# Performance work log

Measured on AMD Instinct MI355X. Metric: run time of the kernel, lower is better.

## Reference

```python
import jax, jax.numpy as jnp
import numpy as np

EMBED_DIM = 256
N_HEADS = 1
NORM_FACTOR = float(np.sqrt(EMBED_DIM / N_HEADS))


def setup_inputs() -> dict:
    key = jax.random.key(0)
    ks = jax.random.split(key, 7)
    B, S, E = 4, 4096, EMBED_DIM
    scale = 1.0 / np.sqrt(E)
    x = jax.random.normal(ks[0], (B, S, E), dtype=jnp.float32)
    Wq = jax.random.normal(ks[1], (E, E), dtype=jnp.float32) * scale
    bq = jax.random.normal(ks[2], (E,), dtype=jnp.float32) * 0.01
    Wk = jax.random.normal(ks[3], (E, E), dtype=jnp.float32) * scale
    bk = jax.random.normal(ks[4], (E,), dtype=jnp.float32) * 0.01
    Wv = jax.random.normal(ks[5], (E, E), dtype=jnp.float32) * scale
    bv = jax.random.normal(ks[6], (E,), dtype=jnp.float32) * 0.01
    return {"x": x, "Wq": Wq, "bq": bq, "Wk": Wk, "bk": bk, "Wv": Wv, "bv": bv}


def reference(x, Wq, bq, Wk, bk, Wv, bv):
    # Linear projections (torch Linear: x @ W.T + b; W here stored as [in, out]-equivalent square)
    q = x @ Wq + bq  # [B, S, E]
    k = x @ Wk + bk  # [B, S, E]
    v = x @ Wv + bv  # [B, S, E]
    # Full attention scores [B, S, S], scaled by sqrt(embed_dim / n_heads)
    attn_scores = jnp.einsum('bse,bte->bst', q, k) / NORM_FACTOR
    attn_dist = jax.nn.softmax(attn_scores, axis=-1)
    pooled = jnp.einsum('bst,bte->bse', attn_dist, v)  # [B, S, E]
    return pooled.mean(axis=1, keepdims=True)  # [B, 1, E]
```

## Files before the change

kernel.cpp:

```cpp
#include <hip/hip_runtime.h>
#include <stdint.h>

#define SS 4096
#define EE 256
#define C2 0.0901684400555602f

typedef __bf16 bf16x8 __attribute__((ext_vector_type(8)));
typedef float  f32x4  __attribute__((ext_vector_type(4)));

#if __has_builtin(__builtin_amdgcn_exp2f)
#define EXP2(x) __builtin_amdgcn_exp2f(x)
#else
#define EXP2(x) exp2f(x)
#endif
#if __has_builtin(__builtin_amdgcn_rcpf)
#define RCP(x) __builtin_amdgcn_rcpf(x)
#else
#define RCP(x) (1.0f / (x))
#endif

__device__ __forceinline__ uint16_t bf16_rn(float f) {
  uint32_t u = __float_as_uint(f);
  uint32_t r = (u + 0x7fffu + ((u >> 16) & 1u)) >> 16;
  return (uint16_t)r;
}
__device__ __forceinline__ float bf2f(uint16_t h) {
  return __uint_as_float(((uint32_t)h) << 16);
}
__device__ __forceinline__ bf16x8 pack_bf8(float4 a, float4 b) {
  union { bf16x8 v; uint16_t u[8]; } r;
  r.u[0] = bf16_rn(a.x); r.u[1] = bf16_rn(a.y);
  r.u[2] = bf16_rn(a.z); r.u[3] = bf16_rn(a.w);
  r.u[4] = bf16_rn(b.x); r.u[5] = bf16_rn(b.y);
  r.u[6] = bf16_rn(b.z); r.u[7] = bf16_rn(b.w);
  return r.v;
}

__device__ __forceinline__ f32x4 mfma16(bf16x8 a, bf16x8 b, f32x4 c) {
  return __builtin_amdgcn_mfma_f32_16x16x32_bf16(a, b, c, 0, 0, 0);
}

template<int R>
__device__ __forceinline__ void stage_tile(const uint16_t* gsrc, char* lds, int tid) {
  constexpr int NPER = (R * 32) / 256;
  const int wave = tid >> 6;
  #pragma unroll
  for (int c = 0; c < NPER; ++c) {
    int chunk = c * 256 + tid;
    int r = chunk >> 5;
    int ccl = (chunk & 31) ^ (r & 31);
    const char* gp = (const char*)gsrc + (r * 32 + ccl) * 16;
    char* lp = lds + (c * 256 + wave * 64) * 16;
    __builtin_amdgcn_global_load_lds(
        (const __attribute__((address_space(1))) uint32_t*)(uintptr_t)gp,
        (__attribute__((address_space(3))) uint32_t*)(uintptr_t)lp,
        16, 0, 0);
  }
}

__device__ __forceinline__ bf16x8 read_frag(const char* lds, int row, int cc) {
  int ccp = cc ^ (row & 31);
  return *(const bf16x8*)(lds + (row * 32 + ccp) * 16);
}

__global__ void prep_kernel(const float* __restrict__ Wq, const float* __restrict__ Wk,
                            const float* __restrict__ Wv, uint16_t* __restrict__ wt,
                            float* __restrict__ zbase, float* __restrict__ out) {
  __shared__ float t[64][65];
  const int bid = blockIdx.x, tid = threadIdx.x;
  if (bid >= 48) {
    int idx = (bid - 48) * 256 + tid;
    float4 z = {0.f, 0.f, 0.f, 0.f};
    if (idx < 8192) ((float4*)zbase)[idx] = z;
    else ((float4*)out)[idx - 8192] = z;
    return;
  }
  const int mat = bid >> 4, tt = bid & 15;
  const int ib = (tt >> 2) * 64, ob = (tt & 3) * 64;
  const float* W = (mat == 0) ? Wq : (mat == 1) ? Wk : Wv;
  #pragma unroll
  for (int p = 0; p < 4; ++p) {
    int idx = p * 256 + tid;
    int r = idx >> 4, c4 = idx & 15;
    float4 f = *(const float4*)&W[(size_t)(ib + r) * 256 + ob + c4 * 4];
    t[r][c4 * 4 + 0] = f.x; t[r][c4 * 4 + 1] = f.y;
    t[r][c4 * 4 + 2] = f.z; t[r][c4 * 4 + 3] = f.w;
  }
  __syncthreads();
  #pragma unroll
  for (int p = 0; p < 4; ++p) {
    int idx = p * 256 + tid;
    int o = idx >> 4, i4 = idx & 15;
    ushort4 u;
    u.x = bf16_rn(t[i4 * 4 + 0][o]);
    u.y = bf16_rn(t[i4 * 4 + 1][o]);
    u.z = bf16_rn(t[i4 * 4 + 2][o]);
    u.w = bf16_rn(t[i4 * 4 + 3][o]);
    *(ushort4*)&wt[((size_t)mat * 256 + ob + o) * 256 + ib + i4 * 4] = u;
  }
}

__global__ __launch_bounds__(256, 2) void qkv_kernel(
    const float* __restrict__ x, const uint16_t* __restrict__ wt,
    const float* __restrict__ bq, const float* __restrict__ bk, const float* __restrict__ bv,
    uint16_t* __restrict__ qo, uint16_t* __restrict__ ko, uint16_t* __restrict__ vo) {
  __shared__ char wsm[2][32768];
  const int tid = threadIdx.x;
  const int lane = tid & 63, wave = tid >> 6, quad = lane >> 4, lr = lane & 15;
  const int m0 = (blockIdx.x >> 2) * 128;
  const int cchunk = blockIdx.x & 3;
  stage_tile<64>(wt + (size_t)(cchunk * 192) * 256, wsm[0], tid);
  const float* ab = x + (size_t)(m0 + wave * 32) * EE;
  bf16x8 a[2][8];
  #pragma unroll
  for (int ms = 0; ms < 2; ++ms)
    #pragma unroll
    for (int f = 0; f < 8; ++f) {
      const float* rp = ab + (size_t)(ms * 16 + lr) * EE + f * 32 + quad * 8;
      a[ms][f] = pack_bf8(*(const float4*)rp, *(const float4*)(rp + 4));
    }
  for (int nc = 0; nc < 3; ++nc) {
    __syncthreads();
    if (nc < 2)
      stage_tile<64>(wt + (size_t)(cchunk * 192 + (nc + 1) * 64) * 256, wsm[(nc + 1) & 1], tid);
    const char* tile = wsm[nc & 1];
    #pragma unroll
    for (int nt = 0; nt < 4; ++nt) {
      const int eg0 = cchunk * 192 + nc * 64 + nt * 16;
      const int mat = eg0 >> 8;
      const int e = (eg0 & 255) + lr;
      const float* bias = (mat == 0) ? bq : (mat == 1) ? bk : bv;
      uint16_t* outp = (mat == 0) ? qo : (mat == 1) ? ko : vo;
      bf16x8 bf[8];
      #pragma unroll
      for (int f = 0; f < 8; ++f) bf[f] = read_frag(tile, nt * 16 + lr, f * 4 + quad);
      f32x4 acc[2] = {};
      #pragma unroll
      for (int f = 0; f < 8; ++f)
        #pragma unroll
        for (int ms = 0; ms < 2; ++ms)
          acc[ms] = mfma16(a[ms][f], bf[f], acc[ms]);
      const float bsv = bias[e];
      #pragma unroll
      for (int ms = 0; ms < 2; ++ms)
        #pragma unroll
        for (int r = 0; r < 4; ++r) {
          int row = m0 + wave * 32 + ms * 16 + quad * 4 + r;
          outp[(size_t)row * EE + e] = bf16_rn(acc[ms][r] + bsv);
        }
    }
  }
}

__global__ __launch_bounds__(256, 2) void scores_l_kernel(
    const uint16_t* __restrict__ q, const uint16_t* __restrict__ k,
    float* __restrict__ lacc) {
  __shared__ char kt[2][32768];
  const int tid = threadIdx.x;
  const int lane = tid & 63, wave = tid >> 6, quad = lane >> 4, lr = lane & 15;
  const int idx = blockIdx.x;
  const int b = idx >> 7, rem = idx & 127, qblk = rem >> 3, kch = rem & 7;
  const uint16_t* qb = q + (size_t)(b * SS + qblk * 256 + wave * 64) * EE;
  const uint16_t* kb = k + (size_t)(b * SS + kch * 512) * EE;
  stage_tile<64>(kb, kt[0], tid);
  bf16x8 a[4][8];
  #pragma unroll
  for (int ms = 0; ms < 4; ++ms)
    #pragma unroll
    for (int f = 0; f < 8; ++f)
      a[ms][f] = *(const bf16x8*)(qb + (size_t)(ms * 16 + lr) * EE + f * 32 + quad * 8);
  float accl[16];
  #pragma unroll
  for (int i = 0; i < 16; ++i) accl[i] = 0.f;
  for (int it = 0; it < 8; ++it) {
    __syncthreads();
    if (it + 1 < 8) stage_tile<64>(kb + (size_t)(it + 1) * 64 * EE, kt[(it + 1) & 1], tid);
    const char* tile = kt[it & 1];
    #pragma unroll
    for (int nt = 0; nt < 4; ++nt) {
      bf16x8 bf[8];
      #pragma unroll
      for (int f = 0; f < 8; ++f) bf[f] = read_frag(tile, nt * 16 + lr, f * 4 + quad);
      f32x4 acc[4] = {};
      #pragma unroll
      for (int f = 0; f < 8; ++f)
        #pragma unroll
        for (int ms = 0; ms < 4; ++ms)
          acc[ms] = mfma16(a[ms][f], bf[f], acc[ms]);
      #pragma unroll
      for (int ms = 0; ms < 4; ++ms)
        #pragma unroll
        for (int r = 0; r < 4; ++r)
          accl[ms * 4 + r] += EXP2(acc[ms][r] * C2);
    }
  }
  #pragma unroll
  for (int d = 1; d < 16; d <<= 1)
    #pragma unroll
    for (int i = 0; i < 16; ++i)
      accl[i] += __shfl_xor(accl[i], d, 64);
  if (lr == 0) {
    float* lp = lacc + b * SS + qblk * 256 + wave * 64;
    #pragma unroll
    for (int ms = 0; ms < 4; ++ms)
      #pragma unroll
      for (int r = 0; r < 4; ++r)
        atomicAdd(&lp[ms * 16 + quad * 4 + r], accl[ms * 4 + r]);
  }
}

__global__ __launch_bounds__(256, 2) void scores_w_kernel(
    const uint16_t* __restrict__ q, const uint16_t* __restrict__ k,
    const float* __restrict__ lacc, float* __restrict__ wacc) {
  __shared__ char qt[2][32768];
  const int tid = threadIdx.x;
  const int lane = tid & 63, wave = tid >> 6, quad = lane >> 4, lr = lane & 15;
  const int idx = blockIdx.x;
  const int b = idx >> 7, rem = idx & 127, kblk = rem >> 3, sch = rem & 7;
  const uint16_t* kb = k + (size_t)(b * SS + kblk * 256 + wave * 64) * EE;
  const uint16_t* qb = q + (size_t)(b * SS + sch * 512) * EE;
  const float* rlb = lacc + b * SS + sch * 512;
  stage_tile<64>(qb, qt[0], tid);
  bf16x8 a[4][8];
  #pragma unroll
  for (int ms = 0; ms < 4; ++ms)
    #pragma unroll
    for (int f = 0; f < 8; ++f)
      a[ms][f] = *(const bf16x8*)(kb + (size_t)(ms * 16 + lr) * EE + f * 32 + quad * 8);
  float accw[16];
  #pragma unroll
  for (int i = 0; i < 16; ++i) accw[i] = 0.f;
  for (int it = 0; it < 8; ++it) {
    __syncthreads();
    if (it + 1 < 8) stage_tile<64>(qb + (size_t)(it + 1) * 64 * EE, qt[(it + 1) & 1], tid);
    const char* tile = qt[it & 1];
    #pragma unroll
    for (int nt = 0; nt < 4; ++nt) {
      float rlv = RCP(rlb[it * 64 + nt * 16 + lr]);
      bf16x8 bf[8];
      #pragma unroll
      for (int f = 0; f < 8; ++f) bf[f] = read_frag(tile, nt * 16 + lr, f * 4 + quad);
      f32x4 acc[4] = {};
      #pragma unroll
      for (int f = 0; f < 8; ++f)
        #pragma unroll
        for (int ms = 0; ms < 4; ++ms)
          acc[ms] = mfma16(a[ms][f], bf[f], acc[ms]);
      #pragma unroll
      for (int ms = 0; ms < 4; ++ms)
        #pragma unroll
        for (int r = 0; r < 4; ++r)
          accw[ms * 4 + r] += EXP2(acc[ms][r] * C2) * rlv;
    }
  }
  #pragma unroll
  for (int d = 1; d < 16; d <<= 1)
    #pragma unroll
    for (int i = 0; i < 16; ++i)
      accw[i] += __shfl_xor(accw[i], d, 64);
  if (lr == 0) {
    float* wp = wacc + b * SS + kblk * 256 + wave * 64;
    #pragma unroll
    for (int ms = 0; ms < 4; ++ms)
      #pragma unroll
      for (int r = 0; r < 4; ++r)
        atomicAdd(&wp[ms * 16 + quad * 4 + r], accw[ms * 4 + r]);
  }
}

__global__ void pool_kernel(const float* __restrict__ wsum, const uint16_t* __restrict__ v,
                            float* __restrict__ out) {
  __shared__ float red[4][256];
  const int b = blockIdx.x >> 6, tc = blockIdx.x & 63;
  const int tq = threadIdx.x >> 6, eg = threadIdx.x & 63;
  float acc[4] = {0.f, 0.f, 0.f, 0.f};
  const float* wp = wsum + b * SS + tc * 64;
  const uint16_t* vp = v + (size_t)(b * SS + tc * 64) * EE + eg * 4;
  #pragma unroll
  for (int t = 0; t < 16; ++t) {
    int row = t * 4 + tq;
    float wv = wp[row];
    ushort4 x4 = *(const ushort4*)(vp + (size_t)row * EE);
    acc[0] += wv * bf2f(x4.x);
    acc[1] += wv * bf2f(x4.y);
    acc[2] += wv * bf2f(x4.z);
    acc[3] += wv * bf2f(x4.w);
  }
  #pragma unroll
  for (int j = 0; j < 4; ++j) red[tq][eg * 4 + j] = acc[j];
  __syncthreads();
  if (tq == 0) {
    const float inv = 1.0f / 4096.0f;
    #pragma unroll
    for (int j = 0; j < 4; ++j) {
      float s = red[0][eg * 4 + j] + red[1][eg * 4 + j] +
                red[2][eg * 4 + j] + red[3][eg * 4 + j];
      atomicAdd(&out[b * 256 + eg * 4 + j], s * inv);
    }
  }
}

extern "C" void kernel_launch(void* const* d_in, const int* in_sizes, int n_in,
                              void* d_out, int out_size, void* d_ws, size_t ws_size,
                              hipStream_t stream) {
  const float* x  = (const float*)d_in[0];
  const float* Wq = (const float*)d_in[1];
  const float* bq = (const float*)d_in[2];
  const float* Wk = (const float*)d_in[3];
  const float* bk = (const float*)d_in[4];
  const float* Wv = (const float*)d_in[5];
  const float* bv = (const float*)d_in[6];

  char* ws = (char*)d_ws;
  uint16_t* qb   = (uint16_t*)(ws);
  uint16_t* kb   = (uint16_t*)(ws + 8388608);
  uint16_t* vb   = (uint16_t*)(ws + 16777216);
  uint16_t* wt   = (uint16_t*)(ws + 25165824);
  float* l_arr   = (float*)(ws + 25559040);
  float* w_arr   = (float*)(ws + 25624576);
  float* out     = (float*)d_out;

  prep_kernel<<<81, 256, 0, stream>>>(Wq, Wk, Wv, wt, l_arr, out);
  qkv_kernel<<<512, 256, 0, stream>>>(x, wt, bq, bk, bv, qb, kb, vb);
  scores_l_kernel<<<512, 256, 0, stream>>>(qb, kb, l_arr);
  scores_w_kernel<<<512, 256, 0, stream>>>(qb, kb, l_arr, w_arr);
  pool_kernel<<<256, 256, 0, stream>>>(w_arr, vb, out);
}
```

Before: 180.6 us.

## Give each wave private double-buffered K/Q tiles to drop block barriers

Replaces the block-shared 64-row LDS tile staging, which needed a __syncthreads per iteration, with per-wave 16-row double buffers filled by the wave itself. Synchronisation becomes explicit s_waitcnt on vmcnt/lgkmcnt, so waves proceed independently and global-to-LDS loads overlap the MFMA work. Each wave now loads the full K/Q stream on its own, so LDS-fill traffic rises fourfold, and correctness depends on hand-coded waitcnt immediates. The scores_w kernel also caches the row-sum vector in LDS instead of reading it from global memory inside the loop.

```diff
diff --git a/kernel.cpp b/kernel.cpp
--- a/kernel.cpp
+++ b/kernel.cpp
@@ -4,6 +4,11 @@
 #define SS 4096
 #define EE 256
 #define C2 0.0901684400555602f
+
+#define VMCNT0 0x0F70
+#define VMCNT8 0x0F78
+#define LGKM0  0xC07F
+#define WAITCNT(imm) __builtin_amdgcn_s_waitcnt(imm)
 
 typedef __bf16 bf16x8 __attribute__((ext_vector_type(8)));
 typedef float  f32x4  __attribute__((ext_vector_type(4)));
@@ -57,9 +62,27 @@
         16, 0, 0);
   }
 }
-
 __device__ __forceinline__ bf16x8 read_frag(const char* lds, int row, int cc) {
   int ccp = cc ^ (row & 31);
+  return *(const bf16x8*)(lds + (row * 32 + ccp) * 16);
+}
+
+__device__ __forceinline__ void stage16(const uint16_t* gsrc, char* lds, int lane) {
+  #pragma unroll
+  for (int c = 0; c < 8; ++c) {
+    int p = c * 64 + lane;
+    int r = p >> 5;
+    int ccl = (p & 31) ^ (r & 7);
+    const char* gp = (const char*)gsrc + (r * 32 + ccl) * 16;
+    char* lp = lds + c * 1024;
+    __builtin_amdgcn_global_load_lds(
+        (const __attribute__((address_space(1))) uint32_t*)(uintptr_t)gp,
+        (__attribute__((address_space(3))) uint32_t*)(uintptr_t)lp,
+        16, 0, 0);
+  }
+}
+__device__ __forceinline__ bf16x8 read_frag16(const char* lds, int row, int cc) {
+  int ccp = cc ^ (row & 7);
   return *(const bf16x8*)(lds + (row * 32 + ccp) * 16);
 }
 
@@ -155,44 +178,46 @@
 __global__ __launch_bounds__(256, 2) void scores_l_kernel(
     const uint16_t* __restrict__ q, const uint16_t* __restrict__ k,
     float* __restrict__ lacc) {
-  __shared__ char kt[2][32768];
+  __shared__ char kt[4][2][8192];
   const int tid = threadIdx.x;
   const int lane = tid & 63, wave = tid >> 6, quad = lane >> 4, lr = lane & 15;
   const int idx = blockIdx.x;
   const int b = idx >> 7, rem = idx & 127, qblk = rem >> 3, kch = rem & 7;
   const uint16_t* qb = q + (size_t)(b * SS + qblk * 256 + wave * 64) * EE;
-  const uint16_t* kb = k + (size_t)(b * SS + kch * 512) * EE;
-  stage_tile<64>(kb, kt[0], tid);
+  const uint16_t* kw = k + (size_t)(b * SS + kch * 512) * EE;
   bf16x8 a[4][8];
   #pragma unroll
   for (int ms = 0; ms < 4; ++ms)
     #pragma unroll
     for (int f = 0; f < 8; ++f)
       a[ms][f] = *(const bf16x8*)(qb + (size_t)(ms * 16 + lr) * EE + f * 32 + quad * 8);
+  stage16(kw, kt[wave][0], lane);
+  stage16(kw + 16 * EE, kt[wave][1], lane);
   float accl[16];
   #pragma unroll
   for (int i = 0; i < 16; ++i) accl[i] = 0.f;
-  for (int it = 0; it < 8; ++it) {
-    __syncthreads();
-    if (it + 1 < 8) stage_tile<64>(kb + (size_t)(it + 1) * 64 * EE, kt[(it + 1) & 1], tid);
-    const char* tile = kt[it & 1];
-    #pragma unroll
-    for (int nt = 0; nt < 4; ++nt) {
-      bf16x8 bf[8];
-      #pragma unroll
-      for (int f = 0; f < 8; ++f) bf[f] = read_frag(tile, nt * 16 + lr, f * 4 + quad);
-      f32x4 acc[4] = {};
-      #pragma unroll
-      for (int f = 0; f < 8; ++f)
-        #pragma unroll
-        for (int ms = 0; ms < 4; ++ms)
-          acc[ms] = mfma16(a[ms][f], bf[f], acc[ms]);
+  #pragma unroll 2
+  for (int t = 0; t < 32; ++t) {
+    if (t == 31) WAITCNT(VMCNT0); else WAITCNT(VMCNT8);
+    const char* tile = kt[wave][t & 1];
+    bf16x8 bf[8];
+    #pragma unroll
+    for (int f = 0; f < 8; ++f) bf[f] = read_frag16(tile, lr, f * 4 + quad);
+    f32x4 acc[4] = {};
+    #pragma unroll
+    for (int f = 0; f < 8; ++f)
       #pragma unroll
       for (int ms = 0; ms < 4; ++ms)
-        #pragma unroll
-        for (int r = 0; r < 4; ++r)
-          accl[ms * 4 + r] += EXP2(acc[ms][r] * C2);
-    }
+        acc[ms] = mfma16(a[ms][f], bf[f], acc[ms]);
+    if (t + 2 < 32) {
+      WAITCNT(LGKM0);
+      stage16(kw + (size_t)(t + 2) * 16 * EE, kt[wave][t & 1], lane);
+    }
+    #pragma unroll
+    for (int ms = 0; ms < 4; ++ms)
+      #pragma unroll
+      for (int r = 0; r < 4; ++r)
+        accl[ms * 4 + r] += EXP2(acc[ms][r] * C2);
   }
   #pragma unroll
   for (int d = 1; d < 16; d <<= 1)
@@ -212,46 +237,51 @@
 __global__ __launch_bounds__(256, 2) void scores_w_kernel(
     const uint16_t* __restrict__ q, const uint16_t* __restrict__ k,
     const float* __restrict__ lacc, float* __restrict__ wacc) {
-  __shared__ char qt[2][32768];
+  __shared__ char qt[4][2][8192];
+  __shared__ float rls[512];
   const int tid = threadIdx.x;
   const int lane = tid & 63, wave = tid >> 6, quad = lane >> 4, lr = lane & 15;
   const int idx = blockIdx.x;
   const int b = idx >> 7, rem = idx & 127, kblk = rem >> 3, sch = rem & 7;
   const uint16_t* kb = k + (size_t)(b * SS + kblk * 256 + wave * 64) * EE;
-  const uint16_t* qb = q + (size_t)(b * SS + sch * 512) * EE;
+  const uint16_t* qw = q + (size_t)(b * SS + sch * 512) * EE;
   const float* rlb = lacc + b * SS + sch * 512;
-  stage_tile<64>(qb, qt[0], tid);
+  ((float2*)rls)[tid] = ((const float2*)rlb)[tid];
   bf16x8 a[4][8];
   #pragma unroll
   for (int ms = 0; ms < 4; ++ms)
     #pragma unroll
     for (int f = 0; f < 8; ++f)
       a[ms][f] = *(const bf16x8*)(kb + (size_t)(ms * 16 + lr) * EE + f * 32 + quad * 8);
+  __syncthreads();
+  stage16(qw, qt[wave][0], lane);
+  stage16(qw + 16 * EE, qt[wave][1], lane);
   float accw[16];
   #pragma unroll
   for (int i = 0; i < 16; ++i) accw[i] = 0.f;
-  for (int it = 0; it < 8; ++it) {
-    __syncthreads();
-    if (it + 1 < 8) stage_tile<64>(qb + (size_t)(it + 1) * 64 * EE, qt[(it + 1) & 1], tid);
-    const char* tile = qt[it & 1];
-    #pragma unroll
-    for (int nt = 0; nt < 4; ++nt) {
-      float rlv = RCP(rlb[it * 64 + nt * 16 + lr]);
-      bf16x8 bf[8];
-      #pragma unroll
-      for (int f = 0; f < 8; ++f) bf[f] = read_frag(tile, nt * 16 + lr, f * 4 + quad);
-      f32x4 acc[4] = {};
-      #pragma unroll
-      for (int f = 0; f < 8; ++f)
-        #pragma unroll
-        for (int ms = 0; ms < 4; ++ms)
-          acc[ms] = mfma16(a[ms][f], bf[f], acc[ms]);
+  #pragma unroll 2
+  for (int t = 0; t < 32; ++t) {
+    if (t == 31) WAITCNT(VMCNT0); else WAITCNT(VMCNT8);
+    const char* tile = qt[wave][t & 1];
+    float rlv = RCP(rls[t * 16 + lr]);
+    bf16x8 bf[8];
+    #pragma unroll
+    for (int f = 0; f < 8; ++f) bf[f] = read_frag16(tile, lr, f * 4 + quad);
+    f32x4 acc[4] = {};
+    #pragma unroll
+    for (int f = 0; f < 8; ++f)
       #pragma unroll
       for (int ms = 0; ms < 4; ++ms)
-        #pragma unroll
-        for (int r = 0; r < 4; ++r)
-          accw[ms * 4 + r] += EXP2(acc[ms][r] * C2) * rlv;
-    }
+        acc[ms] = mfma16(a[ms][f], bf[f], acc[ms]);
+    if (t + 2 < 32) {
+      WAITCNT(LGKM0);
+      stage16(qw + (size_t)(t + 2) * 16 * EE, qt[wave][t & 1], lane);
+    }
+    #pragma unroll
+    for (int ms = 0; ms < 4; ++ms)
+      #pragma unroll
+      for (int r = 0; r < 4; ++r)
+        accw[ms * 4 + r] += EXP2(acc[ms][r] * C2) * rlv;
   }
   #pragma unroll
   for (int d = 1; d < 16; d <<= 1)
```

New measurement: 177.4 us. No clear change (-1.8%).

## Quantize Q and K to FP8 and use scaled MFMA for score kernels

Applied to the files above, without the earlier changes.

The QKV projection now writes Q and K as FP8 e4m3 instead of bf16. The two score passes use the 16x16x128 f8f6f4 scaled MFMA with unit scales, FP8 LDS staging, half-size LDS tiles, a finer key/query split (1024 blocks), and 3 blocks per CU. The aim is to halve Q/K memory and LDS traffic and double matrix throughput in the QK^T passes. The cost is reduced precision in the softmax scores, which may affect accuracy.

```diff
diff --git a/kernel.cpp b/kernel.cpp
--- a/kernel.cpp
+++ b/kernel.cpp
@@ -1,12 +1,15 @@
 #include <hip/hip_runtime.h>
+#include <hip/hip_fp8.h>
 #include <stdint.h>
 
 #define SS 4096
 #define EE 256
 #define C2 0.0901684400555602f
+#define SCALE1 0x7F7F7F7F
 
 typedef __bf16 bf16x8 __attribute__((ext_vector_type(8)));
 typedef float  f32x4  __attribute__((ext_vector_type(4)));
+typedef int    i32x8  __attribute__((ext_vector_type(8)));
 
 #if __has_builtin(__builtin_amdgcn_exp2f)
 #define EXP2(x) __builtin_amdgcn_exp2f(x)
@@ -35,9 +38,21 @@
   r.u[6] = bf16_rn(b.z); r.u[7] = bf16_rn(b.w);
   return r.v;
 }
+__device__ __forceinline__ uint8_t f32_to_e4m3(float x) {
+#if __has_builtin(__builtin_amdgcn_cvt_pk_fp8_f32)
+  return (uint8_t)(__builtin_amdgcn_cvt_pk_fp8_f32(x, 0.f, 0, false) & 0xff);
+#else
+  __hip_fp8_e4m3 h(x);
+  return (uint8_t)h.__x;
+#endif
+}
 
 __device__ __forceinline__ f32x4 mfma16(bf16x8 a, bf16x8 b, f32x4 c) {
   return __builtin_amdgcn_mfma_f32_16x16x32_bf16(a, b, c, 0, 0, 0);
+}
+__device__ __forceinline__ f32x4 mfma128(i32x8 a, i32x8 b, f32x4 c) {
+  return __builtin_amdgcn_mfma_scale_f32_16x16x128_f8f6f4(
+      a, b, c, 0 , 0 , 0, SCALE1, 0, SCALE1);
 }
 
 template<int R>
@@ -57,10 +72,31 @@
         16, 0, 0);
   }
 }
-
 __device__ __forceinline__ bf16x8 read_frag(const char* lds, int row, int cc) {
   int ccp = cc ^ (row & 31);
   return *(const bf16x8*)(lds + (row * 32 + ccp) * 16);
+}
+
+__device__ __forceinline__ void stage_fp8_64(const uint8_t* gsrc, char* lds, int tid) {
+  #pragma unroll
+  for (int c = 0; c < 4; ++c) {
+    int chunk = c * 256 + tid;
+    int r = chunk >> 4;
+    int ccl = (chunk & 15) ^ (r & 15);
+    const char* gp = (const char*)gsrc + (r * 16 + ccl) * 16;
+    char* lp = lds + (c * 256 + (tid >> 6) * 64) * 16;
+    __builtin_amdgcn_global_load_lds(
+        (const __attribute__((address_space(1))) uint32_t*)(uintptr_t)gp,
+        (__attribute__((address_space(3))) uint32_t*)(uintptr_t)lp,
+        16, 0, 0);
+  }
+}
+__device__ __forceinline__ i32x8 read_frag8(const char* lds, int t, int win, int quad) {
+  union { i32x8 v; uint4 q[2]; } r;
+  int cc0 = win * 8 + quad * 2;
+  r.q[0] = *(const uint4*)(lds + (t * 16 + ((cc0 + 0) ^ (t & 15))) * 16);
+  r.q[1] = *(const uint4*)(lds + (t * 16 + ((cc0 + 1) ^ (t & 15))) * 16);
+  return r.v;
 }
 
 __global__ void prep_kernel(const float* __restrict__ Wq, const float* __restrict__ Wk,
@@ -103,7 +139,7 @@
 __global__ __launch_bounds__(256, 2) void qkv_kernel(
     const float* __restrict__ x, const uint16_t* __restrict__ wt,
     const float* __restrict__ bq, const float* __restrict__ bk, const float* __restrict__ bv,
-    uint16_t* __restrict__ qo, uint16_t* __restrict__ ko, uint16_t* __restrict__ vo) {
+    uint8_t* __restrict__ q8, uint8_t* __restrict__ k8, uint16_t* __restrict__ vo) {
   __shared__ char wsm[2][32768];
   const int tid = threadIdx.x;
   const int lane = tid & 63, wave = tid >> 6, quad = lane >> 4, lr = lane & 15;
@@ -130,7 +166,6 @@
       const int mat = eg0 >> 8;
       const int e = (eg0 & 255) + lr;
       const float* bias = (mat == 0) ? bq : (mat == 1) ? bk : bv;
-      uint16_t* outp = (mat == 0) ? qo : (mat == 1) ? ko : vo;
       bf16x8 bf[8];
       #pragma unroll
       for (int f = 0; f < 8; ++f) bf[f] = read_frag(tile, nt * 16 + lr, f * 4 + quad);
@@ -146,47 +181,49 @@
         #pragma unroll
         for (int r = 0; r < 4; ++r) {
           int row = m0 + wave * 32 + ms * 16 + quad * 4 + r;
-          outp[(size_t)row * EE + e] = bf16_rn(acc[ms][r] + bsv);
+          float vl = acc[ms][r] + bsv;
+          if (mat == 2)      vo[(size_t)row * EE + e] = bf16_rn(vl);
+          else if (mat == 1) k8[(size_t)row * EE + e] = f32_to_e4m3(vl);
+          else               q8[(size_t)row * EE + e] = f32_to_e4m3(vl);
         }
     }
   }
 }
 
-__global__ __launch_bounds__(256, 2) void scores_l_kernel(
-    const uint16_t* __restrict__ q, const uint16_t* __restrict__ k,
+__global__ __launch_bounds__(256, 3) void scores_l_kernel(
+    const uint8_t* __restrict__ q8, const uint8_t* __restrict__ k8,
     float* __restrict__ lacc) {
-  __shared__ char kt[2][32768];
+  __shared__ char kt[2][16384];
   const int tid = threadIdx.x;
   const int lane = tid & 63, wave = tid >> 6, quad = lane >> 4, lr = lane & 15;
   const int idx = blockIdx.x;
-  const int b = idx >> 7, rem = idx & 127, qblk = rem >> 3, kch = rem & 7;
-  const uint16_t* qb = q + (size_t)(b * SS + qblk * 256 + wave * 64) * EE;
-  const uint16_t* kb = k + (size_t)(b * SS + kch * 512) * EE;
-  stage_tile<64>(kb, kt[0], tid);
-  bf16x8 a[4][8];
+  const int b = idx >> 8, rem = idx & 255, qblk = rem >> 4, kch = rem & 15;
+  const uint8_t* qb = q8 + (size_t)(b * SS + qblk * 256 + wave * 64) * EE;
+  const uint8_t* kb = k8 + (size_t)(b * SS + kch * 256) * EE;
+  stage_fp8_64(kb, kt[0], tid);
+  i32x8 a[4][2];
   #pragma unroll
   for (int ms = 0; ms < 4; ++ms)
     #pragma unroll
-    for (int f = 0; f < 8; ++f)
-      a[ms][f] = *(const bf16x8*)(qb + (size_t)(ms * 16 + lr) * EE + f * 32 + quad * 8);
+    for (int win = 0; win < 2; ++win)
+      a[ms][win] = *(const i32x8*)(qb + (size_t)(ms * 16 + lr) * EE + win * 128 + quad * 32);
   float accl[16];
   #pragma unroll
   for (int i = 0; i < 16; ++i) accl[i] = 0.f;
-  for (int it = 0; it < 8; ++it) {
+  for (int it = 0; it < 4; ++it) {
     __syncthreads();
-    if (it + 1 < 8) stage_tile<64>(kb + (size_t)(it + 1) * 64 * EE, kt[(it + 1) & 1], tid);
+    if (it + 1 < 4) stage_fp8_64(kb + (size_t)(it + 1) * 64 * EE, kt[(it + 1) & 1], tid);
     const char* tile = kt[it & 1];
     #pragma unroll
     for (int nt = 0; nt < 4; ++nt) {
-      bf16x8 bf[8];
-      #pragma unroll
-      for (int f = 0; f < 8; ++f) bf[f] = read_frag(tile, nt * 16 + lr, f * 4 + quad);
+      i32x8 bf0 = read_frag8(tile, nt * 16 + lr, 0, quad);
+      i32x8 bf1 = read_frag8(tile, nt * 16 + lr, 1, quad);
       f32x4 acc[4] = {};
       #pragma unroll
-      for (int f = 0; f < 8; ++f)
-        #pragma unroll
-        for (int ms = 0; ms < 4; ++ms)
-          acc[ms] = mfma16(a[ms][f], bf[f], acc[ms]);
+      for (int ms = 0; ms < 4; ++ms) {
+        acc[ms] = mfma128(a[ms][0], bf0, acc[ms]);
+        acc[ms] = mfma128(a[ms][1], bf1, acc[ms]);
+      }
       #pragma unroll
       for (int ms = 0; ms < 4; ++ms)
         #pragma unroll
@@ -209,43 +246,43 @@
   }
 }
 
-__global__ __launch_bounds__(256, 2) void scores_w_kernel(
-    const uint16_t* __restrict__ q, const uint16_t* __restrict__ k,
+__global__ __launch_bounds__(256, 3) void scores_w_kernel(
+    const uint8_t* __restrict__ q8, const uint8_t* __restrict__ k8,
     const float* __restrict__ lacc, float* __restrict__ wacc) {
-  __shared__ char qt[2][32768];
+  __shared__ char qt[2][16384];
+  __shared__ float rls[256];
   const int tid = threadIdx.x;
   const int lane = tid & 63, wave = tid >> 6, quad = lane >> 4, lr = lane & 15;
   const int idx = blockIdx.x;
-  const int b = idx >> 7, rem = idx & 127, kblk = rem >> 3, sch = rem & 7;
-  const uint16_t* kb = k + (size_t)(b * SS + kblk * 256 + wave * 64) * EE;
-  const uint16_t* qb = q + (size_t)(b * SS + sch * 512) * EE;
-  const float* rlb = lacc + b * SS + sch * 512;
-  stage_tile<64>(qb, qt[0], tid);
-  bf16x8 a[4][8];
+  const int b = idx >> 8, rem = idx & 255, kblk = rem >> 4, sch = rem & 15;
+  const uint8_t* kb = k8 + (size_t)(b * SS + kblk * 256 + wave * 64) * EE;
+  const uint8_t* qw = q8 + (size_t)(b * SS + sch * 256) * EE;
+  rls[tid] = lacc[b * SS + sch * 256 + tid];
+  stage_fp8_64(qw, qt[0], tid);
+  i32x8 a[4][2];
   #pragma unroll
   for (int ms = 0; ms < 4; ++ms)
     #pragma unroll
-    for (int f = 0; f < 8; ++f)
-      a[ms][f] = *(const bf16x8*)(kb + (size_t)(ms * 16 + lr) * EE + f * 32 + quad * 8);
+    for (int win = 0; win < 2; ++win)
+      a[ms][win] = *(const i32x8*)(kb + (size_t)(ms * 16 + lr) * EE + win * 128 + quad * 32);
   float accw[16];
   #pragma unroll
   for (int i = 0; i < 16; ++i) accw[i] = 0.f;
-  for (int it = 0; it < 8; ++it) {
+  for (int it = 0; it < 4; ++it) {
     __syncthreads();
-    if (it + 1 < 8) stage_tile<64>(qb + (size_t)(it + 1) * 64 * EE, qt[(it + 1) & 1], tid);
+    if (it + 1 < 4) stage_fp8_64(qw + (size_t)(it + 1) * 64 * EE, qt[(it + 1) & 1], tid);
     const char* tile = qt[it & 1];
     #pragma unroll
     for (int nt = 0; nt < 4; ++nt) {
-      float rlv = RCP(rlb[it * 64 + nt * 16 + lr]);
-      bf16x8 bf[8];
-      #pragma unroll
-      for (int f = 0; f < 8; ++f) bf[f] = read_frag(tile, nt * 16 + lr, f * 4 + quad);
+      float rlv = RCP(rls[it * 64 + nt * 16 + lr]);
+      i32x8 bf0 = read_frag8(tile, nt * 16 + lr, 0, quad);
+      i32x8 bf1 = read_frag8(tile, nt * 16 + lr, 1, quad);
       f32x4 acc[4] = {};
       #pragma unroll
-      for (int f = 0; f < 8; ++f)
-        #pragma unroll
-        for (int ms = 0; ms < 4; ++ms)
-          acc[ms] = mfma16(a[ms][f], bf[f], acc[ms]);
+      for (int ms = 0; ms < 4; ++ms) {
+        acc[ms] = mfma128(a[ms][0], bf0, acc[ms]);
+        acc[ms] = mfma128(a[ms][1], bf1, acc[ms]);
+      }
       #pragma unroll
       for (int ms = 0; ms < 4; ++ms)
         #pragma unroll
@@ -312,17 +349,17 @@
   const float* bv = (const float*)d_in[6];
 
   char* ws = (char*)d_ws;
-  uint16_t* qb   = (uint16_t*)(ws);
-  uint16_t* kb   = (uint16_t*)(ws + 8388608);
-  uint16_t* vb   = (uint16_t*)(ws + 16777216);
-  uint16_t* wt   = (uint16_t*)(ws + 25165824);
-  float* l_arr   = (float*)(ws + 25559040);
-  float* w_arr   = (float*)(ws + 25624576);
+  uint8_t*  q8   = (uint8_t*)(ws);
+  uint8_t*  k8   = (uint8_t*)(ws + 4194304);
+  uint16_t* vb   = (uint16_t*)(ws + 8388608);
+  uint16_t* wt   = (uint16_t*)(ws + 16777216);
+  float* l_arr   = (float*)(ws + 17170432);
+  float* w_arr   = (float*)(ws + 17235968);
   float* out     = (float*)d_out;
 
   prep_kernel<<<81, 256, 0, stream>>>(Wq, Wk, Wv, wt, l_arr, out);
-  qkv_kernel<<<512, 256, 0, stream>>>(x, wt, bq, bk, bv, qb, kb, vb);
-  scores_l_kernel<<<512, 256, 0, stream>>>(qb, kb, l_arr);
-  scores_w_kernel<<<512, 256, 0, stream>>>(qb, kb, l_arr, w_arr);
+  qkv_kernel<<<512, 256, 0, stream>>>(x, wt, bq, bk, bv, q8, k8, vb);
+  scores_l_kernel<<<1024, 256, 0, stream>>>(q8, k8, l_arr);
+  scores_w_kernel<<<1024, 256, 0, stream>>>(q8, k8, l_arr, w_arr);
   pool_kernel<<<256, 256, 0, stream>>>(w_arr, vb, out);
 }
```

After: 153.0 us. 1.18x faster.
